# Kernel optimization log

Hardware: AMD Instinct MI355X
Metric: run time of the kernel (lower is better)

## Reference

```python
import jax, jax.numpy as jnp
import numpy as np

NUM_HEADS = 6
WIN = 16
NW = 16   # number of windows sharing one mask (b_ % NW == 0)


def setup_inputs() -> dict:
    key = jax.random.key(0)
    ks = jax.random.split(key, 6)
    b_, n, dim = 256, WIN * WIN, 192
    qkv = jax.random.normal(ks[0], (b_, n, 3 * dim), dtype=jnp.float32)
    rpi = jax.random.randint(ks[1], (n, n), 0, (2 * WIN - 1) * (2 * WIN - 1))
    # additive attention mask per window-group (Swin uses 0 / -100; randn is fine for math)
    mask = jax.random.normal(ks[2], (NW, n, n), dtype=jnp.float32)
    rpb_table = 0.02 * jax.random.normal(ks[3], ((2 * WIN - 1) * (2 * WIN - 1), NUM_HEADS), dtype=jnp.float32)
    proj_w = jax.random.normal(ks[4], (dim, dim), dtype=jnp.float32) * (1.0 / np.sqrt(dim))
    proj_b = jax.random.normal(ks[5], (dim,), dtype=jnp.float32) * 0.01
    return {"qkv": qkv, "rpi": rpi, "mask": mask, "rpb_table": rpb_table,
            "proj_w": proj_w, "proj_b": proj_b}


def reference(qkv, rpi, mask, rpb_table, proj_w, proj_b):
    b_, n, c3 = qkv.shape
    c = c3 // 3
    h = NUM_HEADS
    hd = c // h
    scale = float(hd) ** -0.5
    # (b_, n, 3, h, hd) -> (3, b_, h, n, hd)
    qkv = qkv.reshape(b_, n, 3, h, hd).transpose(2, 0, 3, 1, 4)
    q, k, v = qkv[0] * scale, qkv[1], qkv[2]
    attn = jnp.einsum('bhqd,bhkd->bhqk', q, k)  # [b_, h, n, n]
    # gathered relative position bias: [n, n, h] -> [h, n, n]
    bias = rpb_table[rpi].transpose(2, 0, 1)
    attn = attn + bias[None]
    # add per-window-group mask: [b_//nw, nw, h, n, n]
    nw = mask.shape[0]
    attn = attn.reshape(b_ // nw, nw, h, n, n) + mask[None, :, None]
    attn = attn.reshape(b_, h, n, n)
    attn = jax.nn.softmax(attn, axis=-1)
    x = jnp.einsum('bhqk,bhkd->bhqd', attn, v)  # [b_, h, n, hd]
    x = x.transpose(0, 2, 1, 3).reshape(b_, n, c)
    # nn.Linear: x @ W^T + b
    return x @ proj_w.T + proj_b
```

## Files before the change

kernel.cpp:

```cpp
#include <hip/hip_runtime.h>
#include <hip/hip_bf16.h>

typedef _Float16 f16;
typedef _Float16 f16x2 __attribute__((ext_vector_type(2)));
typedef _Float16 f16x4 __attribute__((ext_vector_type(4)));
typedef _Float16 f16x8 __attribute__((ext_vector_type(8)));
typedef __fp16 h16x2 __attribute__((ext_vector_type(2)));
typedef float f32x4 __attribute__((ext_vector_type(4)));

#define NHEADS 6
#define NTOK 256
#define NWINS 256
#define DIM 192
#define HD 32
#define C3 576
#define LOG2E 1.4426950408889634f
#define SCALE (0.17677669529663687f * LOG2E)

__device__ inline f16x2 pkrtz(float a, float b) {
  h16x2 r = __builtin_amdgcn_cvt_pkrtz(a, b);
  return __builtin_bit_cast(f16x2, r);
}

__global__ __launch_bounds__(256) void prep_cb_kernel(const int* __restrict__ rpi,
                                                      const float* __restrict__ mask,
                                                      const float* __restrict__ rpb,
                                                      float* __restrict__ cb) {
  int idx = blockIdx.x * 256 + threadIdx.x;
  int k = idx & 255;
  int q = (idx >> 8) & 255;
  int t = idx >> 16;
  int h = t % 6;
  int mg = t / 6;
  cb[idx] = (rpb[rpi[(q << 8) | k] * 6 + h] + mask[(mg << 16) | (q << 8) | k]) * LOG2E;
}

__global__ __launch_bounds__(256) void prep_w_kernel(const float* __restrict__ w,
                                                     f16* __restrict__ w16) {
  int i = blockIdx.x * 256 + threadIdx.x;
  if (i < DIM * DIM) w16[i] = (f16)w[i];
}

__device__ inline f16x8 q_to_f16(float4 a, float4 b) {
  f16x2 p0 = pkrtz(a.x * SCALE, a.y * SCALE);
  f16x2 p1 = pkrtz(a.z * SCALE, a.w * SCALE);
  f16x2 p2 = pkrtz(b.x * SCALE, b.y * SCALE);
  f16x2 p3 = pkrtz(b.z * SCALE, b.w * SCALE);
  f16x4 lo = __builtin_shufflevector(p0, p1, 0, 1, 2, 3);
  f16x4 hi = __builtin_shufflevector(p2, p3, 0, 1, 2, 3);
  return __builtin_shufflevector(lo, hi, 0, 1, 2, 3, 4, 5, 6, 7);
}

__global__ __launch_bounds__(512, 4) void attn_kernel(const float* __restrict__ qkv,
                                                      const float* __restrict__ cb,
                                                      f16* __restrict__ x16) {
  const int idx = blockIdx.x;
  const int b = idx & 255;
  const int h = idx >> 8;
  const int tid = threadIdx.x;
  const int lane = tid & 63;
  const int wave = tid >> 6;
  const int g = lane >> 4;
  const int r16 = lane & 15;

  __shared__ f16 Klin[16 * 64 * 8];
  __shared__ f16 VT[32][264];

  {
    const int t = tid & 255;
    const int srow = t >> 3;
    const int part = t & 7;
    const bool isK = tid < 256;
    const float* base = qkv + (size_t)(b * NTOK + srow) * C3 + DIM + (isK ? 0 : DIM)
                        + h * HD + part * 4;
    const int gg = part >> 1;
    const int half = part & 1;
    const int d0 = part * 4;
#pragma unroll
    for (int batch = 0; batch < 2; ++batch) {
      float4 v4[4];
#pragma unroll
      for (int rg = 0; rg < 4; ++rg)
        v4[rg] = *(const float4*)(base + (size_t)((batch * 4 + rg) * 32) * C3);
#pragma unroll
      for (int rg = 0; rg < 4; ++rg) {
        const int row = (batch * 4 + rg) * 32 + srow;
        if (isK) {
          const int slot = ((row >> 4) * 64) + gg * 16 + ((row & 15) ^ (gg << 2));
          f16x2 k01 = pkrtz(v4[rg].x, v4[rg].y);
          f16x2 k23 = pkrtz(v4[rg].z, v4[rg].w);
          *((f16x4*)&Klin[slot * 8 + half * 4]) =
              __builtin_shufflevector(k01, k23, 0, 1, 2, 3);
        } else {
          VT[d0 + 0][row ^ (((d0 + 0) & 7) << 2)] = (f16)v4[rg].x;
          VT[d0 + 1][row ^ (((d0 + 1) & 7) << 2)] = (f16)v4[rg].y;
          VT[d0 + 2][row ^ (((d0 + 2) & 7) << 2)] = (f16)v4[rg].z;
          VT[d0 + 3][row ^ (((d0 + 3) & 7) << 2)] = (f16)v4[rg].w;
        }
      }
    }
  }
  __syncthreads();

  const int qbase = wave * 32;
  const float* cbb = cb + (((size_t)((b & 15) * 6 + h)) << 16);
  const int krd = (lane & 48) + ((lane & 15) ^ ((lane >> 2) & 12));

#pragma unroll
  for (int c = 0; c < 2; ++c) {
    const int qrow = qbase + c * 16 + r16;
    const float* qp = qkv + (size_t)(b * NTOK + qrow) * C3 + h * HD + g * 8;
    f16x8 qf = q_to_f16(((const float4*)qp)[0], ((const float4*)qp)[1]);
    const float* cbq = cbb + ((size_t)qrow << 8) + g * 4;

    f32x4 acc[8];
#pragma unroll
    for (int kt = 0; kt < 8; ++kt)
      acc[kt] = *((const f32x4*)(cbq + kt * 16));
#pragma unroll
    for (int kt = 0; kt < 8; ++kt) {
      f16x8 af = *((const f16x8*)&Klin[(kt * 64 + krd) * 8]);
      acc[kt] = __builtin_amdgcn_mfma_f32_16x16x32_f16(af, qf, acc[kt], 0, 0, 0);
    }

    float m0 = fmaxf(fmaxf(acc[0][0], acc[1][0]), fmaxf(acc[2][0], acc[3][0]));
    float m1 = fmaxf(fmaxf(acc[0][1], acc[1][1]), fmaxf(acc[2][1], acc[3][1]));
    float m2 = fmaxf(fmaxf(acc[0][2], acc[1][2]), fmaxf(acc[2][2], acc[3][2]));
    float m3 = fmaxf(fmaxf(acc[0][3], acc[1][3]), fmaxf(acc[2][3], acc[3][3]));
#pragma unroll
    for (int kt = 4; kt < 8; ++kt) {
      m0 = fmaxf(m0, acc[kt][0]); m1 = fmaxf(m1, acc[kt][1]);
      m2 = fmaxf(m2, acc[kt][2]); m3 = fmaxf(m3, acc[kt][3]);
    }
    float mA = fmaxf(fmaxf(m0, m1), fmaxf(m2, m3));
    mA = fmaxf(mA, __shfl_xor(mA, 16));
    mA = fmaxf(mA, __shfl_xor(mA, 32));

    float s0 = 0.f, s1 = 0.f, s2 = 0.f, s3 = 0.f;
#pragma unroll
    for (int kt = 0; kt < 8; ++kt) {
      float p0 = __builtin_amdgcn_exp2f(acc[kt][0] - mA);
      float p1 = __builtin_amdgcn_exp2f(acc[kt][1] - mA);
      float p2 = __builtin_amdgcn_exp2f(acc[kt][2] - mA);
      float p3 = __builtin_amdgcn_exp2f(acc[kt][3] - mA);
      acc[kt][0] = p0; acc[kt][1] = p1; acc[kt][2] = p2; acc[kt][3] = p3;
      s0 += p0; s1 += p1; s2 += p2; s3 += p3;
    }
    float sA = (s0 + s1) + (s2 + s3);

    f32x4 xa0[2], xa1[2];
#pragma unroll
    for (int dt = 0; dt < 2; ++dt) {
      xa0[dt][0] = 0.f; xa0[dt][1] = 0.f; xa0[dt][2] = 0.f; xa0[dt][3] = 0.f;
      xa1[dt][0] = 0.f; xa1[dt][1] = 0.f; xa1[dt][2] = 0.f; xa1[dt][3] = 0.f;
    }
#pragma unroll
    for (int kt = 0; kt < 8; ++kt) {
      f16x2 p01 = pkrtz(acc[kt][0], acc[kt][1]);
      f16x2 p23 = pkrtz(acc[kt][2], acc[kt][3]);
      f16x4 pf = __builtin_shufflevector(p01, p23, 0, 1, 2, 3);
#pragma unroll
      for (int dt = 0; dt < 2; ++dt) {
        const int col = (kt * 16 + g * 4) ^ ((r16 & 7) << 2);
        f16x4 vf = *((const f16x4*)&VT[dt * 16 + r16][col]);
        if (kt < 4)
          xa0[dt] = __builtin_amdgcn_mfma_f32_16x16x16f16(vf, pf, xa0[dt], 0, 0, 0);
        else
          xa1[dt] = __builtin_amdgcn_mfma_f32_16x16x16f16(vf, pf, xa1[dt], 0, 0, 0);
      }
    }

#pragma unroll
    for (int kt = 0; kt < 8; ++kt)
      acc[kt] = *((const f32x4*)(cbq + 128 + kt * 16));
#pragma unroll
    for (int kt = 0; kt < 8; ++kt) {
      f16x8 af = *((const f16x8*)&Klin[((kt + 8) * 64 + krd) * 8]);
      acc[kt] = __builtin_amdgcn_mfma_f32_16x16x32_f16(af, qf, acc[kt], 0, 0, 0);
    }

    m0 = fmaxf(fmaxf(acc[0][0], acc[1][0]), fmaxf(acc[2][0], acc[3][0]));
    m1 = fmaxf(fmaxf(acc[0][1], acc[1][1]), fmaxf(acc[2][1], acc[3][1]));
    m2 = fmaxf(fmaxf(acc[0][2], acc[1][2]), fmaxf(acc[2][2], acc[3][2]));
    m3 = fmaxf(fmaxf(acc[0][3], acc[1][3]), fmaxf(acc[2][3], acc[3][3]));
#pragma unroll
    for (int kt = 4; kt < 8; ++kt) {
      m0 = fmaxf(m0, acc[kt][0]); m1 = fmaxf(m1, acc[kt][1]);
      m2 = fmaxf(m2, acc[kt][2]); m3 = fmaxf(m3, acc[kt][3]);
    }
    float mB = fmaxf(fmaxf(m0, m1), fmaxf(m2, m3));
    mB = fmaxf(mB, __shfl_xor(mB, 16));
    mB = fmaxf(mB, __shfl_xor(mB, 32));

    const float m = fmaxf(mA, mB);
    const float scA = __builtin_amdgcn_exp2f(mA - m);

    s0 = 0.f; s1 = 0.f; s2 = 0.f; s3 = 0.f;
#pragma unroll
    for (int kt = 0; kt < 8; ++kt) {
      float p0 = __builtin_amdgcn_exp2f(acc[kt][0] - m);
      float p1 = __builtin_amdgcn_exp2f(acc[kt][1] - m);
      float p2 = __builtin_amdgcn_exp2f(acc[kt][2] - m);
      float p3 = __builtin_amdgcn_exp2f(acc[kt][3] - m);
      acc[kt][0] = p0; acc[kt][1] = p1; acc[kt][2] = p2; acc[kt][3] = p3;
      s0 += p0; s1 += p1; s2 += p2; s3 += p3;
    }
    float s = sA * scA + (s0 + s1) + (s2 + s3);
    s += __shfl_xor(s, 16);
    s += __shfl_xor(s, 32);
    const float rinv = 1.0f / s;

#pragma unroll
    for (int dt = 0; dt < 2; ++dt) {
      xa0[dt][0] *= scA; xa0[dt][1] *= scA; xa0[dt][2] *= scA; xa0[dt][3] *= scA;
      xa1[dt][0] *= scA; xa1[dt][1] *= scA; xa1[dt][2] *= scA; xa1[dt][3] *= scA;
    }
#pragma unroll
    for (int kt = 0; kt < 8; ++kt) {
      f16x2 p01 = pkrtz(acc[kt][0], acc[kt][1]);
      f16x2 p23 = pkrtz(acc[kt][2], acc[kt][3]);
      f16x4 pf = __builtin_shufflevector(p01, p23, 0, 1, 2, 3);
#pragma unroll
      for (int dt = 0; dt < 2; ++dt) {
        const int col = ((kt + 8) * 16 + g * 4) ^ ((r16 & 7) << 2);
        f16x4 vf = *((const f16x4*)&VT[dt * 16 + r16][col]);
        if (kt < 4)
          xa0[dt] = __builtin_amdgcn_mfma_f32_16x16x16f16(vf, pf, xa0[dt], 0, 0, 0);
        else
          xa1[dt] = __builtin_amdgcn_mfma_f32_16x16x16f16(vf, pf, xa1[dt], 0, 0, 0);
      }
    }

    f16* xp = x16 + (size_t)(b * NTOK + qrow) * DIM + h * HD;
#pragma unroll
    for (int dt = 0; dt < 2; ++dt) {
      f16x2 o01 = pkrtz((xa0[dt][0] + xa1[dt][0]) * rinv,
                        (xa0[dt][1] + xa1[dt][1]) * rinv);
      f16x2 o23 = pkrtz((xa0[dt][2] + xa1[dt][2]) * rinv,
                        (xa0[dt][3] + xa1[dt][3]) * rinv);
      *((f16x4*)(xp + dt * 16 + g * 4)) = __builtin_shufflevector(o01, o23, 0, 1, 2, 3);
    }
  }
}

__global__ __launch_bounds__(256) void proj_kernel(const f16* __restrict__ x16,
                                                   const f16* __restrict__ w16,
                                                   const float* __restrict__ pb,
                                                   float* __restrict__ out) {
  const int lane = threadIdx.x & 63;
  const int wave = threadIdx.x >> 6;
  const int g = lane >> 4;
  const int r16 = lane & 15;
  const int m0 = blockIdx.x * 64 + wave * 16;

  f32x4 acc[12];
#pragma unroll
  for (int jt = 0; jt < 12; ++jt) {
    acc[jt][0] = 0.f; acc[jt][1] = 0.f; acc[jt][2] = 0.f; acc[jt][3] = 0.f;
  }
#pragma unroll
  for (int cc = 0; cc < 6; ++cc) {
    f16x8 af = *((const f16x8*)(x16 + (size_t)(m0 + r16) * DIM + cc * 32 + g * 8));
#pragma unroll
    for (int jt = 0; jt < 12; ++jt) {
      f16x8 bf = *((const f16x8*)(w16 + (size_t)(jt * 16 + r16) * DIM + cc * 32 + g * 8));
      acc[jt] = __builtin_amdgcn_mfma_f32_16x16x32_f16(af, bf, acc[jt], 0, 0, 0);
    }
  }
#pragma unroll
  for (int jt = 0; jt < 12; ++jt) {
    int j = jt * 16 + r16;
    float bias = pb[j];
#pragma unroll
    for (int r = 0; r < 4; ++r) {
      out[(size_t)(m0 + g * 4 + r) * DIM + j] = acc[jt][r] + bias;
    }
  }
}

extern "C" void kernel_launch(void* const* d_in, const int* in_sizes, int n_in,
                              void* d_out, int out_size, void* d_ws, size_t ws_size,
                              hipStream_t stream) {
  const float* qkv  = (const float*)d_in[0];
  const int*   rpi  = (const int*)d_in[1];
  const float* mask = (const float*)d_in[2];
  const float* rpb  = (const float*)d_in[3];
  const float* pw   = (const float*)d_in[4];
  const float* pbv  = (const float*)d_in[5];
  float* out = (float*)d_out;

  char* ws = (char*)d_ws;
  float* cb = (float*)ws;
  f16* x16  = (f16*)(ws + 25165824);
  f16* w16  = (f16*)(ws + 25165824 + 25165824);

  prep_cb_kernel<<<24576, 256, 0, stream>>>(rpi, mask, rpb, cb);
  prep_w_kernel<<<144, 256, 0, stream>>>(pw, w16);
  attn_kernel<<<1536, 512, 0, stream>>>(qkv, cb, x16);
  proj_kernel<<<1024, 256, 0, stream>>>(x16, w16, pbv, out);
}
```

Baseline: 122.9 us.

## Split combined bias into separate fp16 rpb and mask tables added in-kernel

Replaces the precomputed fp32 combined bias+mask tensor (96 groups × 256×256, ~25MB written then read) with two small fp16 tables: per-head relative-position bias and per-group mask. The attention kernel loads both halves as f16x4, adds them and accumulates into the scores after the MFMA, instead of seeding the accumulator with fp32 bias. This cuts the prep kernel's write traffic and the attention kernel's bias read bandwidth roughly fourfold, at the cost of some extra VALU adds and fp16 rounding of bias and mask.

```diff
diff --git a/kernel.cpp b/kernel.cpp
--- a/kernel.cpp
+++ b/kernel.cpp
@@ -22,17 +22,22 @@
   return __builtin_bit_cast(f16x2, r);
 }
 
-__global__ __launch_bounds__(256) void prep_cb_kernel(const int* __restrict__ rpi,
-                                                      const float* __restrict__ mask,
-                                                      const float* __restrict__ rpb,
-                                                      float* __restrict__ cb) {
+__global__ __launch_bounds__(256) void prep_rpb_kernel(const int* __restrict__ rpi,
+                                                       const float* __restrict__ rpb,
+                                                       f16* __restrict__ rpb16) {
   int idx = blockIdx.x * 256 + threadIdx.x;
-  int k = idx & 255;
-  int q = (idx >> 8) & 255;
-  int t = idx >> 16;
-  int h = t % 6;
-  int mg = t / 6;
-  cb[idx] = (rpb[rpi[(q << 8) | k] * 6 + h] + mask[(mg << 16) | (q << 8) | k]) * LOG2E;
+  int qk = idx & 65535;
+  int h = idx >> 16;
+  rpb16[idx] = (f16)(rpb[rpi[qk] * 6 + h] * LOG2E);
+}
+
+__global__ __launch_bounds__(256) void prep_mask_kernel(const float* __restrict__ mask,
+                                                        f16* __restrict__ mask16) {
+  int i = (blockIdx.x * 256 + threadIdx.x) * 4;
+  float4 v = *(const float4*)(mask + i);
+  f16x2 lo = pkrtz(v.x * LOG2E, v.y * LOG2E);
+  f16x2 hi = pkrtz(v.z * LOG2E, v.w * LOG2E);
+  *((f16x4*)(mask16 + i)) = __builtin_shufflevector(lo, hi, 0, 1, 2, 3);
 }
 
 __global__ __launch_bounds__(256) void prep_w_kernel(const float* __restrict__ w,
@@ -52,7 +57,8 @@
 }
 
 __global__ __launch_bounds__(512, 4) void attn_kernel(const float* __restrict__ qkv,
-                                                      const float* __restrict__ cb,
+                                                      const f16* __restrict__ rpb16,
+                                                      const f16* __restrict__ mask16,
                                                       f16* __restrict__ x16) {
   const int idx = blockIdx.x;
   const int b = idx & 255;
@@ -103,7 +109,8 @@
   __syncthreads();
 
   const int qbase = wave * 32;
-  const float* cbb = cb + (((size_t)((b & 15) * 6 + h)) << 16);
+  const f16* rb = rpb16 + ((size_t)h << 16);
+  const f16* mb = mask16 + ((size_t)(b & 15) << 16);
   const int krd = (lane & 48) + ((lane & 15) ^ ((lane >> 2) & 12));
 
 #pragma unroll
@@ -111,24 +118,33 @@
     const int qrow = qbase + c * 16 + r16;
     const float* qp = qkv + (size_t)(b * NTOK + qrow) * C3 + h * HD + g * 8;
     f16x8 qf = q_to_f16(((const float4*)qp)[0], ((const float4*)qp)[1]);
-    const float* cbq = cbb + ((size_t)qrow << 8) + g * 4;
-
+    const int qoff = (qrow << 8) + g * 4;
+
+    f16x4 rv[8], mv[8];
+#pragma unroll
+    for (int kt = 0; kt < 8; ++kt) {
+      rv[kt] = *((const f16x4*)(rb + qoff + kt * 16));
+      mv[kt] = *((const f16x4*)(mb + qoff + kt * 16));
+    }
     f32x4 acc[8];
 #pragma unroll
-    for (int kt = 0; kt < 8; ++kt)
-      acc[kt] = *((const f32x4*)(cbq + kt * 16));
+    for (int kt = 0; kt < 8; ++kt) {
+      acc[kt][0] = 0.f; acc[kt][1] = 0.f; acc[kt][2] = 0.f; acc[kt][3] = 0.f;
+    }
 #pragma unroll
     for (int kt = 0; kt < 8; ++kt) {
       f16x8 af = *((const f16x8*)&Klin[(kt * 64 + krd) * 8]);
       acc[kt] = __builtin_amdgcn_mfma_f32_16x16x32_f16(af, qf, acc[kt], 0, 0, 0);
     }
 
-    float m0 = fmaxf(fmaxf(acc[0][0], acc[1][0]), fmaxf(acc[2][0], acc[3][0]));
-    float m1 = fmaxf(fmaxf(acc[0][1], acc[1][1]), fmaxf(acc[2][1], acc[3][1]));
-    float m2 = fmaxf(fmaxf(acc[0][2], acc[1][2]), fmaxf(acc[2][2], acc[3][2]));
-    float m3 = fmaxf(fmaxf(acc[0][3], acc[1][3]), fmaxf(acc[2][3], acc[3][3]));
-#pragma unroll
-    for (int kt = 4; kt < 8; ++kt) {
+    float m0 = -1e30f, m1 = -1e30f, m2 = -1e30f, m3 = -1e30f;
+#pragma unroll
+    for (int kt = 0; kt < 8; ++kt) {
+      f16x4 sv = rv[kt] + mv[kt];
+      acc[kt][0] += (float)sv[0];
+      acc[kt][1] += (float)sv[1];
+      acc[kt][2] += (float)sv[2];
+      acc[kt][3] += (float)sv[3];
       m0 = fmaxf(m0, acc[kt][0]); m1 = fmaxf(m1, acc[kt][1]);
       m2 = fmaxf(m2, acc[kt][2]); m3 = fmaxf(m3, acc[kt][3]);
     }
@@ -171,20 +187,28 @@
     }
 
 #pragma unroll
-    for (int kt = 0; kt < 8; ++kt)
-      acc[kt] = *((const f32x4*)(cbq + 128 + kt * 16));
+    for (int kt = 0; kt < 8; ++kt) {
+      rv[kt] = *((const f16x4*)(rb + qoff + 128 + kt * 16));
+      mv[kt] = *((const f16x4*)(mb + qoff + 128 + kt * 16));
+    }
+#pragma unroll
+    for (int kt = 0; kt < 8; ++kt) {
+      acc[kt][0] = 0.f; acc[kt][1] = 0.f; acc[kt][2] = 0.f; acc[kt][3] = 0.f;
+    }
 #pragma unroll
     for (int kt = 0; kt < 8; ++kt) {
       f16x8 af = *((const f16x8*)&Klin[((kt + 8) * 64 + krd) * 8]);
       acc[kt] = __builtin_amdgcn_mfma_f32_16x16x32_f16(af, qf, acc[kt], 0, 0, 0);
     }
 
-    m0 = fmaxf(fmaxf(acc[0][0], acc[1][0]), fmaxf(acc[2][0], acc[3][0]));
-    m1 = fmaxf(fmaxf(acc[0][1], acc[1][1]), fmaxf(acc[2][1], acc[3][1]));
-    m2 = fmaxf(fmaxf(acc[0][2], acc[1][2]), fmaxf(acc[2][2], acc[3][2]));
-    m3 = fmaxf(fmaxf(acc[0][3], acc[1][3]), fmaxf(acc[2][3], acc[3][3]));
-#pragma unroll
-    for (int kt = 4; kt < 8; ++kt) {
+    m0 = -1e30f; m1 = -1e30f; m2 = -1e30f; m3 = -1e30f;
+#pragma unroll
+    for (int kt = 0; kt < 8; ++kt) {
+      f16x4 sv = rv[kt] + mv[kt];
+      acc[kt][0] += (float)sv[0];
+      acc[kt][1] += (float)sv[1];
+      acc[kt][2] += (float)sv[2];
+      acc[kt][3] += (float)sv[3];
       m0 = fmaxf(m0, acc[kt][0]); m1 = fmaxf(m1, acc[kt][1]);
       m2 = fmaxf(m2, acc[kt][2]); m3 = fmaxf(m3, acc[kt][3]);
     }
@@ -290,12 +314,14 @@
   float* out = (float*)d_out;
 
   char* ws = (char*)d_ws;
-  float* cb = (float*)ws;
-  f16* x16  = (f16*)(ws + 25165824);
-  f16* w16  = (f16*)(ws + 25165824 + 25165824);
-
-  prep_cb_kernel<<<24576, 256, 0, stream>>>(rpi, mask, rpb, cb);
+  f16* rpb16  = (f16*)ws;
+  f16* mask16 = (f16*)(ws + 786432);
+  f16* x16    = (f16*)(ws + 786432 + 2097152);
+  f16* w16    = (f16*)(ws + 786432 + 2097152 + 25165824);
+
+  prep_rpb_kernel<<<1536, 256, 0, stream>>>(rpi, rpb, rpb16);
+  prep_mask_kernel<<<1024, 256, 0, stream>>>(mask, mask16);
   prep_w_kernel<<<144, 256, 0, stream>>>(pw, w16);
-  attn_kernel<<<1536, 512, 0, stream>>>(qkv, cb, x16);
+  attn_kernel<<<1536, 512, 0, stream>>>(qkv, rpb16, mask16, x16);
   proj_kernel<<<1024, 256, 0, stream>>>(x16, w16, pbv, out);
 }
```

After: 158.2 us. 28.7% more time.

## Store combined bias/mask table in fp16 with MFMA-friendly layout and regroup blocks

Applied to the files above, without the earlier changes.

The precomputed bias+mask table is stored as fp16 instead of fp32, in an interleaved layout so each lane loads 8 contiguous halves per 128-bit load and widens them into the MFMA accumulators. The attention grid is also remapped so consecutive blocks share the same mask group and head, which improves L2 reuse of the table. This halves the table traffic in both the prep and attention kernels, at the cost of fp16 rounding of the additive bias/mask.

```diff
diff --git a/kernel.cpp b/kernel.cpp
--- a/kernel.cpp
+++ b/kernel.cpp
@@ -25,14 +25,19 @@
 __global__ __launch_bounds__(256) void prep_cb_kernel(const int* __restrict__ rpi,
                                                       const float* __restrict__ mask,
                                                       const float* __restrict__ rpb,
-                                                      float* __restrict__ cb) {
+                                                      f16* __restrict__ cb) {
   int idx = blockIdx.x * 256 + threadIdx.x;
-  int k = idx & 255;
+  int rem = idx & 255;
   int q = (idx >> 8) & 255;
   int t = idx >> 16;
   int h = t % 6;
   int mg = t / 6;
-  cb[idx] = (rpb[rpi[(q << 8) | k] * 6 + h] + mask[(mg << 16) | (q << 8) | k]) * LOG2E;
+  int ktp = rem >> 5;
+  int gg = (rem >> 3) & 3;
+  int e = rem & 7;
+  int k = (2 * ktp + (e >> 2)) * 16 + gg * 4 + (e & 3);
+  float v = (rpb[rpi[(q << 8) | k] * 6 + h] + mask[(mg << 16) | (q << 8) | k]) * LOG2E;
+  cb[idx] = (f16)v;
 }
 
 __global__ __launch_bounds__(256) void prep_w_kernel(const float* __restrict__ w,
@@ -52,11 +57,13 @@
 }
 
 __global__ __launch_bounds__(512, 4) void attn_kernel(const float* __restrict__ qkv,
-                                                      const float* __restrict__ cb,
+                                                      const f16* __restrict__ cb,
                                                       f16* __restrict__ x16) {
   const int idx = blockIdx.x;
-  const int b = idx & 255;
-  const int h = idx >> 8;
+  const int grp = idx % 96;
+  const int jhi = idx / 96;
+  const int b = (jhi << 4) | (grp / 6);
+  const int h = grp % 6;
   const int tid = threadIdx.x;
   const int lane = tid & 63;
   const int wave = tid >> 6;
@@ -103,7 +110,7 @@
   __syncthreads();
 
   const int qbase = wave * 32;
-  const float* cbb = cb + (((size_t)((b & 15) * 6 + h)) << 16);
+  const f16* cbb = cb + ((size_t)grp << 16);
   const int krd = (lane & 48) + ((lane & 15) ^ ((lane >> 2) & 12));
 
 #pragma unroll
@@ -111,12 +118,20 @@
     const int qrow = qbase + c * 16 + r16;
     const float* qp = qkv + (size_t)(b * NTOK + qrow) * C3 + h * HD + g * 8;
     f16x8 qf = q_to_f16(((const float4*)qp)[0], ((const float4*)qp)[1]);
-    const float* cbq = cbb + ((size_t)qrow << 8) + g * 4;
-
+    const f16* cbq = cbb + (qrow << 8) + g * 8;
+
+    f16x8 cv[4];
+#pragma unroll
+    for (int kp = 0; kp < 4; ++kp) cv[kp] = *((const f16x8*)(cbq + kp * 32));
     f32x4 acc[8];
 #pragma unroll
-    for (int kt = 0; kt < 8; ++kt)
-      acc[kt] = *((const f32x4*)(cbq + kt * 16));
+    for (int kp = 0; kp < 4; ++kp) {
+#pragma unroll
+      for (int r = 0; r < 4; ++r) {
+        acc[2 * kp][r] = (float)cv[kp][r];
+        acc[2 * kp + 1][r] = (float)cv[kp][4 + r];
+      }
+    }
 #pragma unroll
     for (int kt = 0; kt < 8; ++kt) {
       f16x8 af = *((const f16x8*)&Klin[(kt * 64 + krd) * 8]);
@@ -171,8 +186,15 @@
     }
 
 #pragma unroll
-    for (int kt = 0; kt < 8; ++kt)
-      acc[kt] = *((const f32x4*)(cbq + 128 + kt * 16));
+    for (int kp = 0; kp < 4; ++kp) cv[kp] = *((const f16x8*)(cbq + 128 + kp * 32));
+#pragma unroll
+    for (int kp = 0; kp < 4; ++kp) {
+#pragma unroll
+      for (int r = 0; r < 4; ++r) {
+        acc[2 * kp][r] = (float)cv[kp][r];
+        acc[2 * kp + 1][r] = (float)cv[kp][4 + r];
+      }
+    }
 #pragma unroll
     for (int kt = 0; kt < 8; ++kt) {
       f16x8 af = *((const f16x8*)&Klin[((kt + 8) * 64 + krd) * 8]);
@@ -290,12 +312,12 @@
   float* out = (float*)d_out;
 
   char* ws = (char*)d_ws;
-  float* cb = (float*)ws;
-  f16* x16  = (f16*)(ws + 25165824);
-  f16* w16  = (f16*)(ws + 25165824 + 25165824);
-
-  prep_cb_kernel<<<24576, 256, 0, stream>>>(rpi, mask, rpb, cb);
+  f16* cb16 = (f16*)ws;
+  f16* x16  = (f16*)(ws + 12582912);
+  f16* w16  = (f16*)(ws + 12582912 + 25165824);
+
+  prep_cb_kernel<<<24576, 256, 0, stream>>>(rpi, mask, rpb, cb16);
   prep_w_kernel<<<144, 256, 0, stream>>>(pw, w16);
-  attn_kernel<<<1536, 512, 0, stream>>>(qkv, cb, x16);
+  attn_kernel<<<1536, 512, 0, stream>>>(qkv, cb16, x16);
   proj_kernel<<<1024, 256, 0, stream>>>(x16, w16, pbv, out);
 }
```

Measured after the change: 110.4 us. 1.11x faster.
